# Optimization experiments

Hardware: AMD Instinct MI355X
Metric: run time of the kernel (lower is better)

The kernel has to match this reference:

```python
import jax, jax.numpy as jnp
import numpy as np

N, B, E = 2048, 2, 1024      # seq_len, batch, embedding_dims
H = 1024                      # hidden_dims
NH, D = 16, 64                # num_heads, head_dim (NH*D == H)
SCALE = 1.0 / float(np.sqrt(H))  # NOTE: module divides by sqrt(hidden_dims), not sqrt(head_dim)


def setup_inputs() -> dict:
    key = jax.random.key(0)
    k0, k1, k2 = jax.random.split(key, 3)
    x = jax.random.normal(k0, (N, B, E), dtype=jnp.float32)
    W_proj = jax.random.normal(k1, (E, 3 * H), dtype=jnp.float32) * 0.02
    b_proj = jnp.zeros((3 * H,), dtype=jnp.float32)
    W_out = jax.random.normal(k2, (H, E), dtype=jnp.float32) * 0.02
    b_out = jnp.zeros((E,), dtype=jnp.float32)
    return {"x": x, "W_proj": W_proj, "b_proj": b_proj, "W_out": W_out, "b_out": b_out}


def reference(x, W_proj, b_proj, W_out, b_out):
    n, b, _ = x.shape
    # QKV projection: [n, b, 3H] -> 'n b (k h d) -> k b h n d'
    proj = x @ W_proj + b_proj
    qkv = proj.reshape(n, b, 3, NH, D).transpose(2, 1, 3, 0, 4)  # [3, b, h, n, d]
    q, k, v = qkv[0], qkv[1], qkv[2]
    # scaled dot-product scores [b, h, n, n]
    scores = jnp.einsum('bhid,bhjd->bhij', q, k) * SCALE
    # causal mask: -inf above the diagonal (generate_square_subsequent_mask)
    i = jnp.arange(n)
    mask = jnp.where(i[None, :] > i[:, None], -jnp.inf, 0.0).astype(scores.dtype)
    att = jax.nn.softmax(scores + mask, axis=-1)  # dropout = identity (eval)
    out = jnp.einsum('bhij,bhjd->bhid', att, v)   # [b, h, n, d]
    out = out.transpose(2, 0, 1, 3).reshape(n, b, H)  # 'b h n d -> n b (h d)'
    return out @ W_out + b_out
```

## Files before the change

kernel.cpp:

```cpp
#include <hip/hip_runtime.h>
#include <cstdint>
#include <cstddef>

typedef __bf16 bf16_t;
typedef __bf16 bf16x8 __attribute__((ext_vector_type(8)));
typedef __bf16 bf16x4 __attribute__((ext_vector_type(4)));
typedef float f32x4 __attribute__((ext_vector_type(4)));

#define N_SEQ 2048
#define BATCH 2
#define EMB   1024
#define HID   1024
#define NHEAD 16
#define HDIM  64
#define NBROW (N_SEQ * BATCH)
#define ATT_SCALE2 (0.03125f * 1.44269504f)

#define EXP2F(x) __builtin_amdgcn_exp2f(x)

static __device__ __forceinline__ void async_copy16(const bf16_t* g, bf16_t* l) {
  __builtin_amdgcn_global_load_lds((const __attribute__((address_space(1))) void*)g,
                                   (__attribute__((address_space(3))) void*)l,
                                   16, 0, 0);
}

__global__ __launch_bounds__(256) void prep_kernel(
    const float* __restrict__ x, const float* __restrict__ Wp,
    const float* __restrict__ Wo, bf16_t* __restrict__ Xb,
    bf16_t* __restrict__ Wpt, bf16_t* __restrict__ Wot) {
  int bid = blockIdx.x;
  if (bid < 4096) {
    int i = (bid * 256 + threadIdx.x) * 4;
    float4 v = *(const float4*)(x + i);
    bf16x4 o;
    o[0] = (bf16_t)v.x; o[1] = (bf16_t)v.y; o[2] = (bf16_t)v.z; o[3] = (bf16_t)v.w;
    *(bf16x4*)(Xb + i) = o;
    return;
  }
  __shared__ float tile[32][33];
  const float* in; bf16_t* out; int R, C, bx;
  if (bid < 4096 + 3072) { bx = bid - 4096; in = Wp; out = Wpt; R = 1024; C = 3072; }
  else                   { bx = bid - 7168; in = Wo; out = Wot; R = 1024; C = 1024; }
  int gx = C / 32;
  int bc = (bx % gx) * 32, br = (bx / gx) * 32;
  int tx = threadIdx.x & 31, ty = threadIdx.x >> 5;
  #pragma unroll
  for (int i = 0; i < 32; i += 8)
    tile[ty + i][tx] = in[(size_t)(br + ty + i) * C + bc + tx];
  __syncthreads();
  #pragma unroll
  for (int i = 0; i < 32; i += 8)
    out[(size_t)(bc + ty + i) * R + br + tx] = (bf16_t)tile[tx][ty + i];
}

template <int BM, int BN, int TPB, bool OUT_BF16, bool SCALEQ, bool WRITE_VT>
__global__ __launch_bounds__(TPB) void gemm_bt_kernel(
    const bf16_t* __restrict__ A, const bf16_t* __restrict__ Bt,
    const float* __restrict__ bias, void* __restrict__ Cout,
    bf16_t* __restrict__ Vt, int M, int Nn, int K) {
  constexpr int BK = 64;
  constexpr int NW = TPB / 64;
  constexpr int WROW = 2, WCOL = NW / 2;
  constexpr int MT = BM / WROW / 16;
  constexpr int NT = BN / WCOL / 16;
  constexpr int CA = BM * 8 / TPB;
  constexpr int CB = BN * 8 / TPB;
  constexpr int ASZ = BM * BK;
  constexpr int BSZ = BN * BK;
  __shared__ __align__(16) bf16_t smem[2 * ASZ + 2 * BSZ];
  bf16_t* const Asb = smem;
  bf16_t* const Bsb = smem + 2 * ASZ;
  int tid = threadIdx.x;
  int wave = tid >> 6, lane = tid & 63;
  int c = lane & 15, quad = lane >> 4;
  int bm = blockIdx.x * BM;
  int bn = blockIdx.y * BN;
  int wm = (wave % WROW) * (BM / WROW);
  int wn = (wave / WROW) * (BN / WCOL);
  f32x4 acc[MT][NT] = {};

  const bf16_t* agp[CA]; int alo[CA];
  const bf16_t* bgp[CB]; int blo[CB];
  #pragma unroll
  for (int i = 0; i < CA; ++i) {
    int p = i * TPB + tid;
    int row = p >> 3, ko = (p & 7) ^ (row & 7);
    agp[i] = A + (size_t)(bm + row) * K + ko * 8;
    alo[i] = (i * TPB + wave * 64) * 8;
  }
  #pragma unroll
  for (int i = 0; i < CB; ++i) {
    int p = i * TPB + tid;
    int row = p >> 3, ko = (p & 7) ^ (row & 7);
    bgp[i] = Bt + (size_t)(bn + row) * K + ko * 8;
    blo[i] = (i * TPB + wave * 64) * 8;
  }

  #pragma unroll
  for (int i = 0; i < CA; ++i) async_copy16(agp[i], Asb + alo[i]);
  #pragma unroll
  for (int i = 0; i < CB; ++i) async_copy16(bgp[i], Bsb + blo[i]);

  int nkb = K / BK;
  for (int ki = 0; ki < nkb; ++ki) {
    __syncthreads();
    if (ki + 1 < nkb) {
      int kb = (ki + 1) * BK;
      bf16_t* an = Asb + ((ki + 1) & 1) * ASZ;
      bf16_t* bnx = Bsb + ((ki + 1) & 1) * BSZ;
      #pragma unroll
      for (int i = 0; i < CA; ++i) async_copy16(agp[i] + kb, an + alo[i]);
      #pragma unroll
      for (int i = 0; i < CB; ++i) async_copy16(bgp[i] + kb, bnx + blo[i]);
    }
    const bf16_t* as = Asb + (ki & 1) * ASZ;
    const bf16_t* bs = Bsb + (ki & 1) * BSZ;
    #pragma unroll
    for (int kk = 0; kk < 2; ++kk) {
      bf16x8 af[MT], bf[NT];
      #pragma unroll
      for (int mt = 0; mt < MT; ++mt) {
        int row = wm + mt * 16 + c;
        int slot = (kk * 4 + quad) ^ (row & 7);
        af[mt] = *(const bf16x8*)(as + (size_t)(row * 8 + slot) * 8);
      }
      #pragma unroll
      for (int nt = 0; nt < NT; ++nt) {
        int row = wn + nt * 16 + c;
        int slot = (kk * 4 + quad) ^ (row & 7);
        bf[nt] = *(const bf16x8*)(bs + (size_t)(row * 8 + slot) * 8);
      }
      #pragma unroll
      for (int mt = 0; mt < MT; ++mt)
        #pragma unroll
        for (int nt = 0; nt < NT; ++nt)
          acc[mt][nt] = __builtin_amdgcn_mfma_f32_16x16x32_bf16(
              af[mt], bf[nt], acc[mt][nt], 0, 0, 0);
    }
  }

  bool do_vt = WRITE_VT && (bn >= 2 * HID);
  bf16_t* tb = smem;
  if (do_vt) __syncthreads();

  #pragma unroll
  for (int nt = 0; nt < NT; ++nt) {
    int col = bn + wn + nt * 16 + c;
    float bv = bias[col];
    float sc = (SCALEQ && col < HID) ? ATT_SCALE2 : 1.0f;
    #pragma unroll
    for (int mt = 0; mt < MT; ++mt) {
      #pragma unroll
      for (int r = 0; r < 4; ++r) {
        int loc = wm + mt * 16 + quad * 4 + r;
        int row = bm + loc;
        float v = (acc[mt][nt][r] + bv) * sc;
        if (OUT_BF16)
          ((bf16_t*)Cout)[(size_t)row * Nn + col] = (bf16_t)v;
        else
          ((float*)Cout)[(size_t)row * Nn + col] = v;
        if (do_vt) {
          int dg = wn + nt * 16 + c;
          int hh = dg >> 6, dl = dg & 63;
          tb[((loc & 1) * 2 + hh) * 4608 + dl * 72 + (loc >> 1)] = (bf16_t)v;
        }
      }
    }
  }

  if (do_vt) {
    __syncthreads();
    int h0 = (bn - 2 * HID) >> 6;
    constexpr int KV = 512 / TPB;
    #pragma unroll
    for (int i = 0; i < 2; ++i) {
      #pragma unroll
      for (int hh = 0; hh < 2; ++hh) {
        #pragma unroll
        for (int k = 0; k < KV; ++k) {
          int idx = k * TPB + tid;
          int d = idx >> 3;
          int n2 = (idx & 7) * 8;
          bf16x8 vv = *(const bf16x8*)(tb + ((i * 2 + hh) * 4608) + d * 72 + n2);
          *(bf16x8*)(Vt + (size_t)((i * 16 + h0 + hh) * HDIM + d) * N_SEQ + bm / 2 + n2) = vv;
        }
      }
    }
  }
}

__global__ __launch_bounds__(512, 4) void flash_attn_kernel(
    const bf16_t* __restrict__ Pj, const bf16_t* __restrict__ Vt,
    bf16_t* __restrict__ AO) {
  __shared__ __align__(16) bf16_t Ks[3][64 * 64];
  __shared__ __align__(16) bf16_t Vs[3][64 * 64];
  __shared__ __align__(16) bf16_t Ps[8][16 * 64];
  const int PJP = 3 * HID;
  int tid = threadIdx.x, wave = tid >> 6, lane = tid & 63;
  int c = lane & 15, quad = lane >> 4;
  int c7 = c & 7;
  int bid = blockIdx.x;
  int qb = (bid < 256) ? (15 - (bid >> 5)) : ((bid - 256) >> 5);
  int bh = bid & 31;
  int h = bh & 15, b = bh >> 4;
  int i0 = qb * 128;

  int i_row = i0 + wave * 16 + c;
  const bf16_t* qg = Pj + (size_t)(i_row * BATCH + b) * PJP + h * HDIM + quad * 8;
  bf16x8 qf0 = *(const bf16x8*)(qg);
  bf16x8 qf1 = *(const bf16x8*)(qg + 32);

  f32x4 o[4] = {};
  float lrow = 0.f;

  int jr = tid >> 3, oc = tid & 7;
  int lds_off = jr * 64 + (oc ^ (jr & 7)) * 8;
  const bf16_t* kg0 = Pj + (size_t)b * PJP + HID + h * HDIM + oc * 8;
  const bf16_t* vg0 = Vt + (size_t)(bh * HDIM + jr) * N_SEQ + oc * 8;

  int njt = 2 * qb + 2;

  bf16x8 kreg = *(const bf16x8*)(kg0 + (size_t)jr * BATCH * PJP);
  bf16x8 vreg = *(const bf16x8*)(vg0);
  *(bf16x8*)(Ks[0] + lds_off) = kreg;
  *(bf16x8*)(Vs[0] + lds_off) = vreg;
  kreg = *(const bf16x8*)(kg0 + (size_t)(64 + jr) * BATCH * PJP);
  vreg = *(const bf16x8*)(vg0 + 64);
  *(bf16x8*)(Ks[1] + lds_off) = kreg;
  *(bf16x8*)(Vs[1] + lds_off) = vreg;
  __syncthreads();

  f32x4 st[4];
  #pragma unroll
  for (int mt = 0; mt < 4; ++mt) {
    const bf16_t* kr = Ks[0] + (mt * 16 + c) * 64;
    bf16x8 ka0 = *(const bf16x8*)(kr + ((quad) ^ c7) * 8);
    bf16x8 ka1 = *(const bf16x8*)(kr + ((quad + 4) ^ c7) * 8);
    f32x4 s = {};
    s = __builtin_amdgcn_mfma_f32_16x16x32_bf16(ka0, qf0, s, 0, 0, 0);
    st[mt] = __builtin_amdgcn_mfma_f32_16x16x32_bf16(ka1, qf1, s, 0, 0, 0);
  }
  if (njt > 2) {
    kreg = *(const bf16x8*)(kg0 + (size_t)(128 + jr) * BATCH * PJP);
    vreg = *(const bf16x8*)(vg0 + 128);
  }

  for (int jt = 0; jt < njt; ++jt) {
    if (jt) __syncthreads();
    if (jt + 2 < njt) {
      *(bf16x8*)(Ks[(jt + 2) % 3] + lds_off) = kreg;
      *(bf16x8*)(Vs[(jt + 2) % 3] + lds_off) = vreg;
    }
    if (jt + 3 < njt) {
      int j0n = (jt + 3) * 64;
      kreg = *(const bf16x8*)(kg0 + (size_t)(j0n + jr) * BATCH * PJP);
      vreg = *(const bf16x8*)(vg0 + j0n);
    }

    f32x4 stN[4];
    bool more = (jt + 1 < njt);
    if (more) {
      const bf16_t* ks = Ks[(jt + 1) % 3];
      #pragma unroll
      for (int mt = 0; mt < 4; ++mt) {
        const bf16_t* kr = ks + (mt * 16 + c) * 64;
        bf16x8 ka0 = *(const bf16x8*)(kr + ((quad) ^ c7) * 8);
        bf16x8 ka1 = *(const bf16x8*)(kr + ((quad + 4) ^ c7) * 8);
        f32x4 s = {};
        s = __builtin_amdgcn_mfma_f32_16x16x32_bf16(ka0, qf0, s, 0, 0, 0);
        stN[mt] = __builtin_amdgcn_mfma_f32_16x16x32_bf16(ka1, qf1, s, 0, 0, 0);
      }
    }

    if (jt >= 2 * qb) {
      int j0 = jt * 64;
      int ig = i0 + wave * 16 + c;
      #pragma unroll
      for (int mt = 0; mt < 4; ++mt)
        #pragma unroll
        for (int r = 0; r < 4; ++r)
          if (j0 + mt * 16 + quad * 4 + r > ig) st[mt][r] = -1e30f;
    }
    #pragma unroll
    for (int mt = 0; mt < 4; ++mt)
      #pragma unroll
      for (int r = 0; r < 4; ++r) {
        st[mt][r] = EXP2F(st[mt][r]);
        lrow += st[mt][r];
      }

    bf16_t* pw = Ps[wave];
    #pragma unroll
    for (int mt = 0; mt < 4; ++mt) {
      bf16x4 pv;
      #pragma unroll
      for (int r = 0; r < 4; ++r) pv[r] = (bf16_t)st[mt][r];
      int joct = mt * 2 + (quad >> 1);
      *(bf16x4*)(pw + c * 64 + (joct ^ c7) * 8 + (quad & 1) * 4) = pv;
    }
    const bf16_t* pr = pw + c * 64;
    bf16x8 pa0 = *(const bf16x8*)(pr + ((quad) ^ c7) * 8);
    bf16x8 pa1 = *(const bf16x8*)(pr + ((quad + 4) ^ c7) * 8);

    const bf16_t* vs = Vs[jt % 3];
    #pragma unroll
    for (int nt = 0; nt < 4; ++nt) {
      const bf16_t* vr = vs + (nt * 16 + c) * 64;
      bf16x8 vb0 = *(const bf16x8*)(vr + ((quad) ^ c7) * 8);
      bf16x8 vb1 = *(const bf16x8*)(vr + ((quad + 4) ^ c7) * 8);
      o[nt] = __builtin_amdgcn_mfma_f32_16x16x32_bf16(vb0, pa0, o[nt], 0, 0, 0);
      o[nt] = __builtin_amdgcn_mfma_f32_16x16x32_bf16(vb1, pa1, o[nt], 0, 0, 0);
    }

    if (more) {
      #pragma unroll
      for (int mt = 0; mt < 4; ++mt) st[mt] = stN[mt];
    }
  }

  float lfull = lrow;
  lfull += __shfl_xor(lfull, 16);
  lfull += __shfl_xor(lfull, 32);
  float linv = 1.0f / lfull;
  int orow = (i0 + wave * 16 + c) * BATCH + b;
  #pragma unroll
  for (int nt = 0; nt < 4; ++nt) {
    bf16x4 pv;
    #pragma unroll
    for (int r = 0; r < 4; ++r) pv[r] = (bf16_t)(o[nt][r] * linv);
    *(bf16x4*)(AO + (size_t)orow * HID + h * HDIM + nt * 16 + quad * 4) = pv;
  }
}

extern "C" void kernel_launch(void* const* d_in, const int* in_sizes, int n_in,
                              void* d_out, int out_size, void* d_ws, size_t ws_size,
                              hipStream_t stream) {
  const float* x      = (const float*)d_in[0];
  const float* W_proj = (const float*)d_in[1];
  const float* b_proj = (const float*)d_in[2];
  const float* W_out  = (const float*)d_in[3];
  const float* b_out  = (const float*)d_in[4];

  bf16_t* Xb  = (bf16_t*)d_ws;
  bf16_t* Wpt = Xb  + (size_t)NBROW * EMB;
  bf16_t* Wot = Wpt + (size_t)3 * HID * EMB;
  bf16_t* Pj  = Wot + (size_t)HID * EMB;
  bf16_t* AO  = Pj  + (size_t)NBROW * 3 * HID;
  bf16_t* Vt  = AO  + (size_t)NBROW * HID;

  prep_kernel<<<8192, 256, 0, stream>>>(x, W_proj, W_out, Xb, Wpt, Wot);
  gemm_bt_kernel<128, 128, 512, true, true, true>
      <<<dim3(NBROW / 128, 3 * HID / 128), 512, 0, stream>>>(
      Xb, Wpt, b_proj, (void*)Pj, Vt, NBROW, 3 * HID, EMB);
  flash_attn_kernel<<<512, 512, 0, stream>>>(Pj, Vt, AO);
  gemm_bt_kernel<128, 64, 256, false, false, false>
      <<<dim3(NBROW / 128, EMB / 64), 256, 0, stream>>>(
      AO, Wot, b_out, d_out, nullptr, NBROW, EMB, HID);
}
```

Measured before the change: 157.3 us.

## Split heavy causal query blocks across two KV halves with a combine pass

The largest causal query blocks (qb 8-15) are split into two workgroups that each process half of the KV range. They write unnormalized fp32 partial outputs and row sums to a workspace, and a new combine kernel sums and normalizes them into AO. Bit-packed lookup tables drive a reordered block schedule across 768 blocks, aimed at reducing tail imbalance in the causal attention. The cost is an extra kernel launch, fp32 partial traffic through global memory, and extra workspace. Skipping the running-max correction works only because softmax here uses no max subtraction.

```diff
diff --git a/kernel.cpp b/kernel.cpp
--- a/kernel.cpp
+++ b/kernel.cpp
@@ -191,7 +191,7 @@
 
 __global__ __launch_bounds__(512, 4) void flash_attn_kernel(
     const bf16_t* __restrict__ Pj, const bf16_t* __restrict__ Vt,
-    bf16_t* __restrict__ AO) {
+    bf16_t* __restrict__ AO, float* __restrict__ OP, float* __restrict__ Lp) {
   __shared__ __align__(16) bf16_t Ks[3][64 * 64];
   __shared__ __align__(16) bf16_t Vs[3][64 * 64];
   __shared__ __align__(16) bf16_t Ps[8][16 * 64];
@@ -200,8 +200,16 @@
   int c = lane & 15, quad = lane >> 4;
   int c7 = c & 7;
   int bid = blockIdx.x;
-  int qb = (bid < 256) ? (15 - (bid >> 5)) : ((bid - 256) >> 5);
-  int bh = bid & 31;
+
+  int g = bid >> 5, bh = bid & 31;
+  int qb = (g < 16) ? ((int)(0x9AA5BBCC6DDEE7FFull >> (4 * g)) & 15)
+                    : ((int)(0x01238849u >> (4 * (g - 16))) & 15);
+  bool heavy = (0xDEF7Bu >> g) & 1;
+  int part = (0x94A52u >> g) & 1;
+  int jt0 = (heavy && part) ? (qb + 1) : 0;
+  int jt1 = heavy ? (part ? (2 * qb + 2) : (qb + 1)) : (2 * qb + 2);
+  int nt_iters = jt1 - jt0;
+
   int h = bh & 15, b = bh >> 4;
   int i0 = qb * 128;
 
@@ -218,14 +226,12 @@
   const bf16_t* kg0 = Pj + (size_t)b * PJP + HID + h * HDIM + oc * 8;
   const bf16_t* vg0 = Vt + (size_t)(bh * HDIM + jr) * N_SEQ + oc * 8;
 
-  int njt = 2 * qb + 2;
-
-  bf16x8 kreg = *(const bf16x8*)(kg0 + (size_t)jr * BATCH * PJP);
-  bf16x8 vreg = *(const bf16x8*)(vg0);
+  bf16x8 kreg = *(const bf16x8*)(kg0 + (size_t)(jt0 * 64 + jr) * BATCH * PJP);
+  bf16x8 vreg = *(const bf16x8*)(vg0 + jt0 * 64);
   *(bf16x8*)(Ks[0] + lds_off) = kreg;
   *(bf16x8*)(Vs[0] + lds_off) = vreg;
-  kreg = *(const bf16x8*)(kg0 + (size_t)(64 + jr) * BATCH * PJP);
-  vreg = *(const bf16x8*)(vg0 + 64);
+  kreg = *(const bf16x8*)(kg0 + (size_t)((jt0 + 1) * 64 + jr) * BATCH * PJP);
+  vreg = *(const bf16x8*)(vg0 + (jt0 + 1) * 64);
   *(bf16x8*)(Ks[1] + lds_off) = kreg;
   *(bf16x8*)(Vs[1] + lds_off) = vreg;
   __syncthreads();
@@ -240,27 +246,28 @@
     s = __builtin_amdgcn_mfma_f32_16x16x32_bf16(ka0, qf0, s, 0, 0, 0);
     st[mt] = __builtin_amdgcn_mfma_f32_16x16x32_bf16(ka1, qf1, s, 0, 0, 0);
   }
-  if (njt > 2) {
-    kreg = *(const bf16x8*)(kg0 + (size_t)(128 + jr) * BATCH * PJP);
-    vreg = *(const bf16x8*)(vg0 + 128);
-  }
-
-  for (int jt = 0; jt < njt; ++jt) {
-    if (jt) __syncthreads();
-    if (jt + 2 < njt) {
-      *(bf16x8*)(Ks[(jt + 2) % 3] + lds_off) = kreg;
-      *(bf16x8*)(Vs[(jt + 2) % 3] + lds_off) = vreg;
-    }
-    if (jt + 3 < njt) {
+  if (nt_iters > 2) {
+    kreg = *(const bf16x8*)(kg0 + (size_t)((jt0 + 2) * 64 + jr) * BATCH * PJP);
+    vreg = *(const bf16x8*)(vg0 + (jt0 + 2) * 64);
+  }
+
+  for (int t = 0; t < nt_iters; ++t) {
+    int jt = jt0 + t;
+    if (t) __syncthreads();
+    if (t + 2 < nt_iters) {
+      *(bf16x8*)(Ks[(t + 2) % 3] + lds_off) = kreg;
+      *(bf16x8*)(Vs[(t + 2) % 3] + lds_off) = vreg;
+    }
+    if (t + 3 < nt_iters) {
       int j0n = (jt + 3) * 64;
       kreg = *(const bf16x8*)(kg0 + (size_t)(j0n + jr) * BATCH * PJP);
       vreg = *(const bf16x8*)(vg0 + j0n);
     }
 
     f32x4 stN[4];
-    bool more = (jt + 1 < njt);
+    bool more = (t + 1 < nt_iters);
     if (more) {
-      const bf16_t* ks = Ks[(jt + 1) % 3];
+      const bf16_t* ks = Ks[(t + 1) % 3];
       #pragma unroll
       for (int mt = 0; mt < 4; ++mt) {
         const bf16_t* kr = ks + (mt * 16 + c) * 64;
@@ -302,7 +309,7 @@
     bf16x8 pa0 = *(const bf16x8*)(pr + ((quad) ^ c7) * 8);
     bf16x8 pa1 = *(const bf16x8*)(pr + ((quad + 4) ^ c7) * 8);
 
-    const bf16_t* vs = Vs[jt % 3];
+    const bf16_t* vs = Vs[t % 3];
     #pragma unroll
     for (int nt = 0; nt < 4; ++nt) {
       const bf16_t* vr = vs + (nt * 16 + c) * 64;
@@ -321,15 +328,43 @@
   float lfull = lrow;
   lfull += __shfl_xor(lfull, 16);
   lfull += __shfl_xor(lfull, 32);
-  float linv = 1.0f / lfull;
   int orow = (i0 + wave * 16 + c) * BATCH + b;
-  #pragma unroll
-  for (int nt = 0; nt < 4; ++nt) {
-    bf16x4 pv;
-    #pragma unroll
-    for (int r = 0; r < 4; ++r) pv[r] = (bf16_t)(o[nt][r] * linv);
-    *(bf16x4*)(AO + (size_t)orow * HID + h * HDIM + nt * 16 + quad * 4) = pv;
-  }
+
+  if (!heavy) {
+    float linv = 1.0f / lfull;
+    #pragma unroll
+    for (int nt = 0; nt < 4; ++nt) {
+      bf16x4 pv;
+      #pragma unroll
+      for (int r = 0; r < 4; ++r) pv[r] = (bf16_t)(o[nt][r] * linv);
+      *(bf16x4*)(AO + (size_t)orow * HID + h * HDIM + nt * 16 + quad * 4) = pv;
+    }
+  } else {
+    float* op = OP + (size_t)part * NBROW * HID + (size_t)orow * HID + h * HDIM;
+    #pragma unroll
+    for (int nt = 0; nt < 4; ++nt)
+      *(f32x4*)(op + nt * 16 + quad * 4) = o[nt];
+    if (lane < 16)
+      Lp[part * 32 * N_SEQ + bh * N_SEQ + (i0 + wave * 16 + c)] = lfull;
+  }
+}
+
+__global__ __launch_bounds__(256) void combine_kernel(
+    const float* __restrict__ OP, const float* __restrict__ Lp,
+    bf16_t* __restrict__ AO) {
+  int gid = blockIdx.x * 256 + threadIdx.x;
+  int col = (gid & 255) * 4;
+  int row = 2048 + (gid >> 8);
+  int i = row >> 1, b = row & 1;
+  int bh = b * 16 + (col >> 6);
+  f32x4 a = *(const f32x4*)(OP + (size_t)row * HID + col);
+  f32x4 c2 = *(const f32x4*)(OP + (size_t)NBROW * HID + (size_t)row * HID + col);
+  float l = Lp[bh * N_SEQ + i] + Lp[32 * N_SEQ + bh * N_SEQ + i];
+  float rinv = 1.0f / l;
+  bf16x4 o;
+  #pragma unroll
+  for (int r = 0; r < 4; ++r) o[r] = (bf16_t)((a[r] + c2[r]) * rinv);
+  *(bf16x4*)(AO + (size_t)row * HID + col) = o;
 }
 
 extern "C" void kernel_launch(void* const* d_in, const int* in_sizes, int n_in,
@@ -347,12 +382,15 @@
   bf16_t* Pj  = Wot + (size_t)HID * EMB;
   bf16_t* AO  = Pj  + (size_t)NBROW * 3 * HID;
   bf16_t* Vt  = AO  + (size_t)NBROW * HID;
+  float*  OP  = (float*)(Vt + (size_t)32 * HDIM * N_SEQ);
+  float*  Lp  = OP + (size_t)2 * NBROW * HID;
 
   prep_kernel<<<8192, 256, 0, stream>>>(x, W_proj, W_out, Xb, Wpt, Wot);
   gemm_bt_kernel<128, 128, 512, true, true, true>
       <<<dim3(NBROW / 128, 3 * HID / 128), 512, 0, stream>>>(
       Xb, Wpt, b_proj, (void*)Pj, Vt, NBROW, 3 * HID, EMB);
-  flash_attn_kernel<<<512, 512, 0, stream>>>(Pj, Vt, AO);
+  flash_attn_kernel<<<768, 512, 0, stream>>>(Pj, Vt, AO, OP, Lp);
+  combine_kernel<<<2048, 256, 0, stream>>>(OP, Lp, AO);
   gemm_bt_kernel<128, 64, 256, false, false, false>
       <<<dim3(NBROW / 128, EMB / 64), 256, 0, stream>>>(
       AO, Wot, b_out, d_out, nullptr, NBROW, EMB, HID);
```

Result: slower. 167.4 us (+6.4%).
